# Optimization experiments

Measured on AMD Instinct MI355X. Metric: run time of the kernel, lower is better.

Reference implementation:

```python
import jax, jax.numpy as jnp
import numpy as np

B, D, H, E, K = 4096, 2048, 2048, 8, 2

def setup_inputs() -> dict:
    key = jax.random.key(0)
    k1, k2, k3 = jax.random.split(key, 3)
    x = jax.random.normal(k1, (B, D), dtype=jnp.float32)
    # keras RandomNormal(stddev=0.001) init for gating and expert kernels, zero bias
    Wg = jax.random.normal(k2, (D, E), dtype=jnp.float32) * 0.001
    bg = jnp.zeros((E,), dtype=jnp.float32)
    We = jax.random.normal(k3, (E, D, H), dtype=jnp.float32) * 0.001
    be = jnp.zeros((E, H), dtype=jnp.float32)
    return {"x": x, "Wg": Wg, "bg": bg, "We": We, "be": be}

def reference(x, Wg, bg, We, be):
    # softmax gating: [B, E]
    gating = jax.nn.softmax(x @ Wg + bg, axis=-1)
    # top-k expert selection
    topk_w, topk_idx = jax.lax.top_k(gating, K)        # [B, K]
    # dense expert stack (module runs all experts): [B, E, H]
    expert_out = jnp.einsum('bd,edh->beh', x, We) + be[None, :, :]
    # gather_nd equivalent: pick top-k experts per token -> [B, K, H]
    topk_out = jnp.take_along_axis(expert_out, topk_idx[:, :, None], axis=1)
    # weighted combine: [B, H]
    combined = jnp.sum(topk_out * topk_w[:, :, None], axis=1)
    return combined
```

## Files before the change

### kernel.cpp

```cpp
#include <hip/hip_runtime.h>
#include <hip/hip_bf16.h>
#include <stdint.h>
#include <stddef.h>

#define B_TOK 4096
#define D_DIM 2048
#define H_DIM 2048
#define E_NUM 8
#define MAX_SLOTS 72

typedef __bf16 bf16;
typedef __attribute__((ext_vector_type(8))) __bf16 bf16x8;
typedef __attribute__((ext_vector_type(4))) __bf16 bf16x4;
typedef __attribute__((ext_vector_type(4))) float f32x4;

#define WS_COUNTS   0
#define WS_ENTRIES  4096
#define WS_TKIDX    135168
#define WS_TKW      167936
#define WS_XBF      262144
#define WS_WET      17039360
#define WS_BIG_NEED 84148224ULL

__device__ __forceinline__ void gload16(const void* g, void* l) {
  __builtin_amdgcn_global_load_lds(
      (const __attribute__((address_space(1))) void*)g,
      (__attribute__((address_space(3))) void*)l, 16, 0, 0);
}

__global__ void zero_counts(int* counts) {
  counts[threadIdx.x] = 0;
}

__global__ __launch_bounds__(256) void gating_kernel(
    const float* __restrict__ x,
    const float* __restrict__ Wg,
    const float* __restrict__ bg,
    int* __restrict__ tk_idx, float* __restrict__ tk_w,
    bf16* __restrict__ xbf,
    const float* __restrict__ be,
    float* __restrict__ out) {
  int gtid = blockIdx.x * blockDim.x + threadIdx.x;
  int b = gtid >> 6;
  int lane = threadIdx.x & 63;
  if (b >= B_TOK) return;
  const float* xrow = x + (size_t)b * D_DIM;

  double acc[E_NUM];
#pragma unroll
  for (int e = 0; e < E_NUM; e++) acc[e] = 0.0;

#pragma unroll
  for (int i = 0; i < 8; i++) {
    int d0 = i * 256 + lane * 4;
    f32x4 xv = *(const f32x4*)(xrow + d0);
    if (xbf) {
      bf16x4 xb;
#pragma unroll
      for (int j = 0; j < 4; j++) xb[j] = (bf16)xv[j];
      *(bf16x4*)(xbf + (size_t)b * D_DIM + d0) = xb;
    }
#pragma unroll
    for (int j = 0; j < 4; j++) {
      double xf = (double)xv[j];
      f32x4 w0 = *(const f32x4*)(Wg + (size_t)(d0 + j) * E_NUM);
      f32x4 w1 = *(const f32x4*)(Wg + (size_t)(d0 + j) * E_NUM + 4);
#pragma unroll
      for (int e = 0; e < 4; e++) acc[e] += xf * (double)w0[e];
#pragma unroll
      for (int e = 0; e < 4; e++) acc[4 + e] += xf * (double)w1[e];
    }
  }
#pragma unroll
  for (int e = 0; e < E_NUM; e++) {
    double v = acc[e];
#pragma unroll
    for (int off = 32; off >= 1; off >>= 1) v += __shfl_xor(v, off, 64);
    acc[e] = v;
  }

  int e0 = 0, e1 = 0;
  float w0f = 0.f, w1f = 0.f;
  if (lane == 0) {
    double lg[E_NUM];
#pragma unroll
    for (int e = 0; e < E_NUM; e++) lg[e] = acc[e] + (double)bg[e];
    int i0 = 0; double v0 = lg[0];
#pragma unroll
    for (int e = 1; e < E_NUM; e++) if (lg[e] > v0) { v0 = lg[e]; i0 = e; }
    int i1 = -1; double v1 = -1e300;
#pragma unroll
    for (int e = 0; e < E_NUM; e++)
      if (e != i0 && lg[e] > v1) { v1 = lg[e]; i1 = e; }
    double m = v0;
    double den = 0.0, p0 = 0.0, p1 = 0.0;
#pragma unroll
    for (int e = 0; e < E_NUM; e++) {
      double pe = exp(lg[e] - m);
      den += pe;
      if (e == i0) p0 = pe;
      if (e == i1) p1 = pe;
    }
    e0 = i0; e1 = i1;
    w0f = (float)(p0 / den);
    w1f = (float)(p1 / den);
    tk_idx[2 * b] = e0;
    tk_idx[2 * b + 1] = e1;
    tk_w[2 * b] = w0f;
    tk_w[2 * b + 1] = w1f;
  }
  e0 = __shfl(e0, 0, 64);
  e1 = __shfl(e1, 0, 64);
  w0f = __shfl(w0f, 0, 64);
  w1f = __shfl(w1f, 0, 64);

  const float* be0 = be + (size_t)e0 * H_DIM;
  const float* be1 = be + (size_t)e1 * H_DIM;
  float* orow = out + (size_t)b * H_DIM;
#pragma unroll
  for (int c = 0; c < 8; c++) {
    int h = c * 256 + lane * 4;
    f32x4 v0 = *(const f32x4*)(be0 + h);
    f32x4 v1 = *(const f32x4*)(be1 + h);
    f32x4 o;
#pragma unroll
    for (int j = 0; j < 4; j++) o[j] = w0f * v0[j] + w1f * v1[j];
    *(f32x4*)(orow + h) = o;
  }
}

__global__ __launch_bounds__(256) void bucketize_kernel(
    const int* __restrict__ tk_idx, int* counts, int* entries) {
  __shared__ int cursor_s;
  __shared__ int base_s;
  int e = blockIdx.x >> 3, chunk = blockIdx.x & 7;
  int tid = threadIdx.x;
  if (tid == 0) cursor_s = 0;
  __syncthreads();

  int flat[4]; bool m[4]; int nm = 0;
#pragma unroll
  for (int j = 0; j < 4; j++) {
    flat[j] = chunk * 1024 + j * 256 + tid;
    int ee = tk_idx[flat[j]];
    m[j] = (ee == e);
    nm += m[j] ? 1 : 0;
  }
  int my_off = atomicAdd(&cursor_s, nm);
  __syncthreads();
  if (tid == 0) base_s = atomicAdd(&counts[e * 16], cursor_s);
  __syncthreads();
  int p = base_s + my_off;
#pragma unroll
  for (int j = 0; j < 4; j++)
    if (m[j]) entries[e * B_TOK + p++] = flat[j];
}

__global__ void transpose_cvt_we(const float* __restrict__ We, bf16* __restrict__ WeT) {
  __shared__ __align__(16) float tile[64][65];
  int e = blockIdx.z;
  int h0 = blockIdx.x * 64, d0 = blockIdx.y * 64;
  int t = threadIdx.x;
  int dr = t >> 2, hc = (t & 3) * 16;
  const float* src = We + ((size_t)e * D_DIM + d0 + dr) * H_DIM + h0 + hc;
#pragma unroll
  for (int i = 0; i < 4; i++)
    *(f32x4*)(&tile[dr][hc + 4 * i]) = *(const f32x4*)(src + 4 * i);
  __syncthreads();
  int lane = t & 63, w = t >> 6;
#pragma unroll
  for (int s = 0; s < 2; s++) {
    int c = w * 2 + s;
    int n16 = c & 3, kslab = c >> 2;
    int nl = n16 * 16 + (lane & 15);
    int kl = kslab * 32 + (lane >> 4) * 8;
    bf16x8 v;
#pragma unroll
    for (int j = 0; j < 8; j++) v[j] = (bf16)tile[kl + j][nl];
    int gh = h0 + nl, gd = d0 + kl;
    int ntile = gh >> 7, n = gh & 127;
    int k0 = gd >> 5;
    size_t slab = ((size_t)((e * 16 + ntile) * 64 + k0)) * 4096;
    int off = ((n >> 4) * 512) + lane * 8;
    *(bf16x8*)(WeT + slab + off) = v;
  }
}

__global__ __launch_bounds__(256) void moe_gemm_fast(
    const bf16* __restrict__ xbf, const bf16* __restrict__ WeT,
    const int* __restrict__ counts, const int* __restrict__ entries,
    const float* __restrict__ tk_w, float* __restrict__ out) {
  __shared__ __align__(16) bf16 As_s[3 * 4096];
  __shared__ __align__(16) bf16 Bs_s[3 * 4096];
  int bid = blockIdx.x;
  int slot = bid >> 4, ntile = bid & 15;
  int e = -1, toff = 0, cnt = 0;
  {
    int tot = 0;
#pragma unroll
    for (int i = 0; i < E_NUM; i++) {
      int c = counts[i * 16];
      int t = (c + 127) >> 7;
      if (slot >= tot && slot < tot + t) { e = i; toff = tot; cnt = c; }
      tot += t;
    }
  }
  if (e < 0) return;
  int mtile = slot - toff;
  int n0 = ntile * 128;
  int tid = threadIdx.x, lane = tid & 63, w = tid >> 6;
  int r = lane & 15, q = lane >> 4;
  const int* ereg = entries + e * B_TOK;
  const bf16* wet_nt = WeT + ((size_t)(e * 16 + ntile) * 64) * 4096;

  const bf16* srcA[2];
  const bf16* srcB[2];
  int chunk_off[2];
#pragma unroll
  for (int j = 0; j < 2; j++) {
    int ci = w * 2 + j;
    int m = mtile * 128 + 16 * ci + r;
    int tok = ereg[min(m, cnt - 1)] >> 1;
    srcA[j] = xbf + (size_t)tok * D_DIM + 8 * q;
    chunk_off[j] = ci * 512;
    srcB[j] = wet_nt + chunk_off[j] + lane * 8;
  }
  int wm4 = (w & 1) * 4, wn4 = (w >> 1) * 4;

  f32x4 acc[4][4];
#pragma unroll
  for (int i = 0; i < 4; i++)
#pragma unroll
    for (int j = 0; j < 4; j++) acc[i][j] = (f32x4){0.f, 0.f, 0.f, 0.f};

#pragma unroll
  for (int p = 0; p < 2; p++) {
#pragma unroll
    for (int j = 0; j < 2; j++) {
      gload16(srcA[j] + p * 32, As_s + p * 4096 + chunk_off[j]);
      gload16(srcB[j] + p * 4096, Bs_s + p * 4096 + chunk_off[j]);
    }
  }

  int pc = 0, pb = 2;
  for (int it = 0; it < 63; it++) {
    asm volatile("s_waitcnt vmcnt(4)\n\ts_barrier" ::: "memory");
    if (it < 62) {
      int kk = (it + 2) * 32;
#pragma unroll
      for (int j = 0; j < 2; j++) {
        gload16(srcA[j] + kk, As_s + pb * 4096 + chunk_off[j]);
        gload16(srcB[j] + (size_t)(it + 2) * 4096, Bs_s + pb * 4096 + chunk_off[j]);
      }
    }
    {
      const bf16* Ab = As_s + pc * 4096;
      const bf16* Bb = Bs_s + pc * 4096;
      bf16x8 af[4], bfr[4];
#pragma unroll
      for (int i = 0; i < 4; i++)
        af[i] = *(const bf16x8*)(Ab + (wm4 + i) * 512 + lane * 8);
#pragma unroll
      for (int j = 0; j < 4; j++)
        bfr[j] = *(const bf16x8*)(Bb + (wn4 + j) * 512 + lane * 8);
#pragma unroll
      for (int i = 0; i < 4; i++)
#pragma unroll
        for (int j = 0; j < 4; j++)
          acc[i][j] = __builtin_amdgcn_mfma_f32_16x16x32_bf16(af[i], bfr[j],
                                                              acc[i][j], 0, 0, 0);
    }
    pc = (pc == 2) ? 0 : pc + 1;
    pb = (pb == 2) ? 0 : pb + 1;
  }
  asm volatile("s_waitcnt vmcnt(0)\n\ts_barrier" ::: "memory");
  {
    const bf16* Ab = As_s + pc * 4096;
    const bf16* Bb = Bs_s + pc * 4096;
    bf16x8 af[4], bfr[4];
#pragma unroll
    for (int i = 0; i < 4; i++)
      af[i] = *(const bf16x8*)(Ab + (wm4 + i) * 512 + lane * 8);
#pragma unroll
    for (int j = 0; j < 4; j++)
      bfr[j] = *(const bf16x8*)(Bb + (wn4 + j) * 512 + lane * 8);
#pragma unroll
    for (int i = 0; i < 4; i++)
#pragma unroll
      for (int j = 0; j < 4; j++)
        acc[i][j] = __builtin_amdgcn_mfma_f32_16x16x32_bf16(af[i], bfr[j],
                                                            acc[i][j], 0, 0, 0);
  }

  int base_r = mtile * 128, wm = (w & 1) * 64, wn = (w >> 1) * 64;
#pragma unroll
  for (int i = 0; i < 4; i++)
#pragma unroll
    for (int reg = 0; reg < 4; reg++) {
      int rg = base_r + wm + 16 * i + q * 4 + reg;
      if (rg < cnt) {
        int ent = ereg[rg];
        int tok = ent >> 1, slotk = ent & 1;
        float wgt = tk_w[2 * tok + slotk];
        float* orow = out + (size_t)tok * H_DIM + n0 + wn;
#pragma unroll
        for (int j = 0; j < 4; j++)
          atomicAdd(orow + 16 * j + r, wgt * acc[i][j][reg]);
      }
    }
}

__global__ __launch_bounds__(256) void moe_gemm_slow(
    const float* __restrict__ x, const float* __restrict__ We,
    const int* __restrict__ counts, const int* __restrict__ entries,
    const float* __restrict__ tk_w, float* __restrict__ out) {
  __shared__ __align__(16) bf16 As_f[4096];
  __shared__ __align__(16) bf16 Bs_f[4096];
  __shared__ __align__(16) float Braw[4096];
  int e = blockIdx.y >> 5, mtile = blockIdx.y & 31;
  int cnt = counts[e * 16];
  if (mtile * 128 >= cnt) return;
  int n0 = blockIdx.x * 128;
  int tid = threadIdx.x, lane = tid & 63, w = tid >> 6;
  int r = lane & 15, q = lane >> 4;
  const int* ereg = entries + e * B_TOK;

  const float* srcA[2]; bf16* dstA[2];
#pragma unroll
  for (int s = 0; s < 2; s++) {
    int c = tid + s * 256;
    int ci = c >> 6, qq = (c >> 4) & 3, rr = c & 15;
    int m = mtile * 128 + 16 * ci + rr;
    int tok = ereg[min(m, cnt - 1)] >> 1;
    srcA[s] = x + (size_t)tok * D_DIM + 8 * qq;
    dstA[s] = As_f + c * 8;
  }
  const float* srcBr[4]; float* dstBr[4];
#pragma unroll
  for (int i = 0; i < 4; i++) {
    int row = (w * 4 + i) * 2 + (lane >> 5);
    srcBr[i] = We + ((size_t)e * D_DIM + row) * H_DIM + n0 + (lane & 31) * 4;
    dstBr[i] = Braw + (w * 4 + i) * 256;
  }
  int n2[2], q2[2]; bf16* dstB2[2];
#pragma unroll
  for (int s = 0; s < 2; s++) {
    int c = tid + s * 256;
    n2[s] = 16 * (c >> 6) + (c & 15);
    q2[s] = (c >> 4) & 3;
    dstB2[s] = Bs_f + c * 8;
  }
  int wm4 = (w & 1) * 4, wn4 = (w >> 1) * 4;

  f32x4 acc[4][4];
#pragma unroll
  for (int i = 0; i < 4; i++)
#pragma unroll
    for (int j = 0; j < 4; j++) acc[i][j] = (f32x4){0.f, 0.f, 0.f, 0.f};

  for (int k0 = 0; k0 < D_DIM; k0 += 32) {
    __syncthreads();
#pragma unroll
    for (int i = 0; i < 4; i++)
      gload16(srcBr[i] + (size_t)k0 * H_DIM, dstBr[i]);
#pragma unroll
    for (int s = 0; s < 2; s++) {
      f32x4 a0 = *(const f32x4*)(srcA[s] + k0);
      f32x4 a1 = *(const f32x4*)(srcA[s] + k0 + 4);
      bf16x8 av;
#pragma unroll
      for (int j = 0; j < 4; j++) { av[j] = (bf16)a0[j]; av[4 + j] = (bf16)a1[j]; }
      *(bf16x8*)dstA[s] = av;
    }
    __syncthreads();
#pragma unroll
    for (int s = 0; s < 2; s++) {
      bf16x8 bv;
#pragma unroll
      for (int t2 = 0; t2 < 8; t2++)
        bv[t2] = (bf16)Braw[(8 * q2[s] + t2) * 128 + n2[s]];
      *(bf16x8*)dstB2[s] = bv;
    }
    __syncthreads();
    bf16x8 af[4], bfr[4];
#pragma unroll
    for (int i = 0; i < 4; i++)
      af[i] = *(const bf16x8*)(As_f + (wm4 + i) * 512 + lane * 8);
#pragma unroll
    for (int j = 0; j < 4; j++)
      bfr[j] = *(const bf16x8*)(Bs_f + (wn4 + j) * 512 + lane * 8);
#pragma unroll
    for (int i = 0; i < 4; i++)
#pragma unroll
      for (int j = 0; j < 4; j++)
        acc[i][j] = __builtin_amdgcn_mfma_f32_16x16x32_bf16(af[i], bfr[j],
                                                            acc[i][j], 0, 0, 0);
  }

  int base_r = mtile * 128, wm = (w & 1) * 64, wn = (w >> 1) * 64;
#pragma unroll
  for (int i = 0; i < 4; i++)
#pragma unroll
    for (int reg = 0; reg < 4; reg++) {
      int rg = base_r + wm + 16 * i + q * 4 + reg;
      if (rg < cnt) {
        int ent = ereg[rg];
        int tok = ent >> 1, slotk = ent & 1;
        float wgt = tk_w[2 * tok + slotk];
        float* orow = out + (size_t)tok * H_DIM + n0 + wn;
#pragma unroll
        for (int j = 0; j < 4; j++)
          atomicAdd(orow + 16 * j + r, wgt * acc[i][j][reg]);
      }
    }
}

extern "C" void kernel_launch(void* const* d_in, const int* in_sizes, int n_in,
                              void* d_out, int out_size, void* d_ws, size_t ws_size,
                              hipStream_t stream) {
  const float* x  = (const float*)d_in[0];
  const float* Wg = (const float*)d_in[1];
  const float* bg = (const float*)d_in[2];
  const float* We = (const float*)d_in[3];
  const float* be = (const float*)d_in[4];
  float* out = (float*)d_out;

  char* ws = (char*)d_ws;
  int*   counts   = (int*)(ws + WS_COUNTS);
  int*   entries  = (int*)(ws + WS_ENTRIES);
  int*   tk_idx   = (int*)(ws + WS_TKIDX);
  float* tk_w     = (float*)(ws + WS_TKW);
  bf16*  xbf      = (bf16*)(ws + WS_XBF);
  bf16*  WeT      = (bf16*)(ws + WS_WET);

  bool big = (ws_size >= WS_BIG_NEED);

  hipLaunchKernelGGL(zero_counts, dim3(1), dim3(128), 0, stream, counts);
  hipLaunchKernelGGL(gating_kernel, dim3(B_TOK / 4), dim3(256), 0, stream,
                     x, Wg, bg, tk_idx, tk_w,
                     big ? xbf : (bf16*)nullptr, be, out);
  hipLaunchKernelGGL(bucketize_kernel, dim3(64), dim3(256), 0, stream,
                     tk_idx, counts, entries);
  if (big) {
    hipLaunchKernelGGL(transpose_cvt_we, dim3(H_DIM / 64, D_DIM / 64, E_NUM),
                       dim3(256), 0, stream, We, WeT);
    hipLaunchKernelGGL(moe_gemm_fast, dim3(MAX_SLOTS * 16), dim3(256), 0, stream,
                       xbf, WeT, counts, entries, tk_w, out);
  } else {
    hipLaunchKernelGGL(moe_gemm_slow, dim3(H_DIM / 128, E_NUM * 32), dim3(256), 0,
                       stream, x, We, counts, entries, tk_w, out);
  }
}
```

Measured before the change: 437.4 us.

## Replace atomic output accumulation with split slot buffers and combine pass; gating in fp32

Gating now runs in fp32 instead of double and no longer converts x or prefills the output. The x conversion and bias prefill move into separate kernels. When the workspace is large enough, the expert GEMM writes each token's two top-k contributions with plain stores into two buffers (out and aux), and a combine kernel then adds them together with the bias. This removes the global atomics and the prefill write, but adds an extra full-size buffer and an extra read/write pass. Switching gating to fp32 risks different top-k picks on near ties.

```diff
diff --git a/kernel.cpp b/kernel.cpp
--- a/kernel.cpp
+++ b/kernel.cpp
@@ -20,7 +20,9 @@
 #define WS_TKW      167936
 #define WS_XBF      262144
 #define WS_WET      17039360
+#define WS_AUX      84148224ULL
 #define WS_BIG_NEED 84148224ULL
+#define WS_SPLIT_NEED 117702656ULL
 
 __device__ __forceinline__ void gload16(const void* g, void* l) {
   __builtin_amdgcn_global_load_lds(
@@ -32,101 +34,99 @@
   counts[threadIdx.x] = 0;
 }
 
-__global__ __launch_bounds__(256) void gating_kernel(
+
+__global__ __launch_bounds__(256) void gating_dot(
     const float* __restrict__ x,
     const float* __restrict__ Wg,
     const float* __restrict__ bg,
-    int* __restrict__ tk_idx, float* __restrict__ tk_w,
-    bf16* __restrict__ xbf,
-    const float* __restrict__ be,
-    float* __restrict__ out) {
+    int* __restrict__ tk_idx, float* __restrict__ tk_w) {
   int gtid = blockIdx.x * blockDim.x + threadIdx.x;
   int b = gtid >> 6;
   int lane = threadIdx.x & 63;
   if (b >= B_TOK) return;
   const float* xrow = x + (size_t)b * D_DIM;
 
-  double acc[E_NUM];
-#pragma unroll
-  for (int e = 0; e < E_NUM; e++) acc[e] = 0.0;
+  float acc[E_NUM];
+#pragma unroll
+  for (int e = 0; e < E_NUM; e++) acc[e] = 0.f;
 
 #pragma unroll
   for (int i = 0; i < 8; i++) {
     int d0 = i * 256 + lane * 4;
     f32x4 xv = *(const f32x4*)(xrow + d0);
-    if (xbf) {
-      bf16x4 xb;
-#pragma unroll
-      for (int j = 0; j < 4; j++) xb[j] = (bf16)xv[j];
-      *(bf16x4*)(xbf + (size_t)b * D_DIM + d0) = xb;
-    }
 #pragma unroll
     for (int j = 0; j < 4; j++) {
-      double xf = (double)xv[j];
+      float xf = xv[j];
       f32x4 w0 = *(const f32x4*)(Wg + (size_t)(d0 + j) * E_NUM);
       f32x4 w1 = *(const f32x4*)(Wg + (size_t)(d0 + j) * E_NUM + 4);
 #pragma unroll
-      for (int e = 0; e < 4; e++) acc[e] += xf * (double)w0[e];
-#pragma unroll
-      for (int e = 0; e < 4; e++) acc[4 + e] += xf * (double)w1[e];
+      for (int e = 0; e < 4; e++) acc[e] += xf * w0[e];
+#pragma unroll
+      for (int e = 0; e < 4; e++) acc[4 + e] += xf * w1[e];
     }
   }
 #pragma unroll
   for (int e = 0; e < E_NUM; e++) {
-    double v = acc[e];
+    float v = acc[e];
 #pragma unroll
     for (int off = 32; off >= 1; off >>= 1) v += __shfl_xor(v, off, 64);
     acc[e] = v;
   }
 
-  int e0 = 0, e1 = 0;
-  float w0f = 0.f, w1f = 0.f;
   if (lane == 0) {
-    double lg[E_NUM];
-#pragma unroll
-    for (int e = 0; e < E_NUM; e++) lg[e] = acc[e] + (double)bg[e];
-    int i0 = 0; double v0 = lg[0];
+    float lg[E_NUM];
+#pragma unroll
+    for (int e = 0; e < E_NUM; e++) lg[e] = acc[e] + bg[e];
+    int i0 = 0; float v0 = lg[0];
 #pragma unroll
     for (int e = 1; e < E_NUM; e++) if (lg[e] > v0) { v0 = lg[e]; i0 = e; }
-    int i1 = -1; double v1 = -1e300;
+    int i1 = -1; float v1 = -1e30f;
 #pragma unroll
     for (int e = 0; e < E_NUM; e++)
       if (e != i0 && lg[e] > v1) { v1 = lg[e]; i1 = e; }
-    double m = v0;
-    double den = 0.0, p0 = 0.0, p1 = 0.0;
+    float m = v0;
+    float den = 0.f, p0 = 0.f, p1 = 0.f;
 #pragma unroll
     for (int e = 0; e < E_NUM; e++) {
-      double pe = exp(lg[e] - m);
+      float pe = expf(lg[e] - m);
       den += pe;
       if (e == i0) p0 = pe;
       if (e == i1) p1 = pe;
     }
-    e0 = i0; e1 = i1;
-    w0f = (float)(p0 / den);
-    w1f = (float)(p1 / den);
-    tk_idx[2 * b] = e0;
-    tk_idx[2 * b + 1] = e1;
-    tk_w[2 * b] = w0f;
-    tk_w[2 * b + 1] = w1f;
-  }
-  e0 = __shfl(e0, 0, 64);
-  e1 = __shfl(e1, 0, 64);
-  w0f = __shfl(w0f, 0, 64);
-  w1f = __shfl(w1f, 0, 64);
-
-  const float* be0 = be + (size_t)e0 * H_DIM;
-  const float* be1 = be + (size_t)e1 * H_DIM;
-  float* orow = out + (size_t)b * H_DIM;
-#pragma unroll
-  for (int c = 0; c < 8; c++) {
-    int h = c * 256 + lane * 4;
-    f32x4 v0 = *(const f32x4*)(be0 + h);
-    f32x4 v1 = *(const f32x4*)(be1 + h);
-    f32x4 o;
-#pragma unroll
-    for (int j = 0; j < 4; j++) o[j] = w0f * v0[j] + w1f * v1[j];
-    *(f32x4*)(orow + h) = o;
-  }
+    tk_idx[2 * b] = i0;
+    tk_idx[2 * b + 1] = i1;
+    tk_w[2 * b] = p0 / den;
+    tk_w[2 * b + 1] = p1 / den;
+  }
+}
+
+__global__ __launch_bounds__(256) void xcvt_kernel(const float* __restrict__ x,
+                                                   bf16* __restrict__ xbf) {
+  int idx = blockIdx.x * blockDim.x + threadIdx.x;
+  f32x4 a = *(const f32x4*)(x + (size_t)idx * 8);
+  f32x4 c = *(const f32x4*)(x + (size_t)idx * 8 + 4);
+  bf16x8 o;
+#pragma unroll
+  for (int j = 0; j < 4; j++) { o[j] = (bf16)a[j]; o[4 + j] = (bf16)c[j]; }
+  *(bf16x8*)(xbf + (size_t)idx * 8) = o;
+}
+
+__global__ __launch_bounds__(256) void prefill_kernel(
+    const float* __restrict__ be,
+    const int* __restrict__ tk_idx,
+    const float* __restrict__ tk_w,
+    float* __restrict__ out) {
+  int idx = blockIdx.x * blockDim.x + threadIdx.x;
+  int b = idx >> 9;
+  int hc = (idx & 511) * 4;
+  int e0 = tk_idx[2 * b], e1 = tk_idx[2 * b + 1];
+  float w0 = tk_w[2 * b], w1 = tk_w[2 * b + 1];
+  f32x4 b0 = *(const f32x4*)(be + (size_t)e0 * H_DIM + hc);
+  f32x4 b1 = *(const f32x4*)(be + (size_t)e1 * H_DIM + hc);
+  f32x4 o;
+#pragma unroll
+  for (int j = 0; j < 4; j++) o[j] = w0 * b0[j] + w1 * b1[j];
+  *(f32x4*)(out + (size_t)b * H_DIM + hc) = o;
 }
 
 __global__ __launch_bounds__(256) void bucketize_kernel(
@@ -189,7 +189,8 @@
 __global__ __launch_bounds__(256) void moe_gemm_fast(
     const bf16* __restrict__ xbf, const bf16* __restrict__ WeT,
     const int* __restrict__ counts, const int* __restrict__ entries,
-    const float* __restrict__ tk_w, float* __restrict__ out) {
+    const float* __restrict__ tk_w, float* __restrict__ out,
+    float* __restrict__ aux) {
   __shared__ __align__(16) bf16 As_s[3 * 4096];
   __shared__ __align__(16) bf16 Bs_s[3 * 4096];
   int bid = blockIdx.x;
@@ -302,12 +303,46 @@
         int ent = ereg[rg];
         int tok = ent >> 1, slotk = ent & 1;
         float wgt = tk_w[2 * tok + slotk];
-        float* orow = out + (size_t)tok * H_DIM + n0 + wn;
-#pragma unroll
-        for (int j = 0; j < 4; j++)
-          atomicAdd(orow + 16 * j + r, wgt * acc[i][j][reg]);
+        if (aux) {
+          float* dst = (slotk ? aux : out) + (size_t)tok * H_DIM + n0 + wn;
+#pragma unroll
+          for (int j = 0; j < 4; j++)
+            dst[16 * j + r] = wgt * acc[i][j][reg];
+        } else {
+          float* orow = out + (size_t)tok * H_DIM + n0 + wn;
+#pragma unroll
+          for (int j = 0; j < 4; j++)
+            atomicAdd(orow + 16 * j + r, wgt * acc[i][j][reg]);
+        }
       }
     }
+}
+
+__global__ __launch_bounds__(256) void combine_kernel(
+    const float* __restrict__ aux,
+    const float* __restrict__ be,
+    const int* __restrict__ tk_idx,
+    const float* __restrict__ tk_w,
+    float* __restrict__ out) {
+  int w = threadIdx.x >> 6, lane = threadIdx.x & 63;
+  int b = blockIdx.x * 4 + w;
+  int e0 = tk_idx[2 * b], e1 = tk_idx[2 * b + 1];
+  float w0 = tk_w[2 * b], w1 = tk_w[2 * b + 1];
+  const float* be0 = be + (size_t)e0 * H_DIM;
+  const float* be1 = be + (size_t)e1 * H_DIM;
+  const float* arow = aux + (size_t)b * H_DIM;
+  float* orow = out + (size_t)b * H_DIM;
+#pragma unroll
+  for (int c = 0; c < 8; c++) {
+    int h = c * 256 + lane * 4;
+    f32x4 o = *(const f32x4*)(orow + h);
+    f32x4 a = *(const f32x4*)(arow + h);
+    f32x4 v0 = *(const f32x4*)(be0 + h);
+    f32x4 v1 = *(const f32x4*)(be1 + h);
+#pragma unroll
+    for (int j = 0; j < 4; j++) o[j] = o[j] + a[j] + w0 * v0[j] + w1 * v1[j];
+    *(f32x4*)(orow + h) = o;
+  }
 }
 
 __global__ __launch_bounds__(256) void moe_gemm_slow(
@@ -432,21 +467,33 @@
   float* tk_w     = (float*)(ws + WS_TKW);
   bf16*  xbf      = (bf16*)(ws + WS_XBF);
   bf16*  WeT      = (bf16*)(ws + WS_WET);
-
-  bool big = (ws_size >= WS_BIG_NEED);
+  float* aux      = (float*)(ws + WS_AUX);
+
+  bool big   = (ws_size >= WS_BIG_NEED);
+  bool split = (ws_size >= WS_SPLIT_NEED);
 
   hipLaunchKernelGGL(zero_counts, dim3(1), dim3(128), 0, stream, counts);
-  hipLaunchKernelGGL(gating_kernel, dim3(B_TOK / 4), dim3(256), 0, stream,
-                     x, Wg, bg, tk_idx, tk_w,
-                     big ? xbf : (bf16*)nullptr, be, out);
+  hipLaunchKernelGGL(gating_dot, dim3(B_TOK / 4), dim3(256), 0, stream,
+                     x, Wg, bg, tk_idx, tk_w);
   hipLaunchKernelGGL(bucketize_kernel, dim3(64), dim3(256), 0, stream,
                      tk_idx, counts, entries);
   if (big) {
+    hipLaunchKernelGGL(xcvt_kernel, dim3(B_TOK * D_DIM / 8 / 256), dim3(256), 0,
+                       stream, x, xbf);
+    if (!split)
+      hipLaunchKernelGGL(prefill_kernel, dim3(B_TOK * H_DIM / 4 / 256), dim3(256),
+                         0, stream, be, tk_idx, tk_w, out);
     hipLaunchKernelGGL(transpose_cvt_we, dim3(H_DIM / 64, D_DIM / 64, E_NUM),
                        dim3(256), 0, stream, We, WeT);
     hipLaunchKernelGGL(moe_gemm_fast, dim3(MAX_SLOTS * 16), dim3(256), 0, stream,
-                       xbf, WeT, counts, entries, tk_w, out);
+                       xbf, WeT, counts, entries, tk_w, out,
+                       split ? aux : (float*)nullptr);
+    if (split)
+      hipLaunchKernelGGL(combine_kernel, dim3(B_TOK / 4), dim3(256), 0, stream,
+                         aux, be, tk_idx, tk_w, out);
   } else {
+    hipLaunchKernelGGL(prefill_kernel, dim3(B_TOK * H_DIM / 4 / 256), dim3(256),
+                       0, stream, be, tk_idx, tk_w, out);
     hipLaunchKernelGGL(moe_gemm_slow, dim3(H_DIM / 128, E_NUM * 32), dim3(256), 0,
                        stream, x, We, counts, entries, tk_w, out);
   }
```

After: 434.8 us. About the same (-0.6%).
